# Optimization experiments

Hardware: AMD Instinct MI355X
Metric: run time of the kernel (lower is better)

Reference implementation:

```python
import jax, jax.numpy as jnp
import numpy as np

B, T, C = 4, 2048, 1024
NH = 16
HD = C // NH
ROPE_BASE = 10000.0


def setup_inputs() -> dict:
    key = jax.random.key(0)
    k1, k2, k3, k4, k5 = jax.random.split(key, 5)
    s = 1.0 / np.sqrt(C)
    return {
        "x": jax.random.normal(k1, (B, T, C), dtype=jnp.float32),
        "W_qkv": jax.random.normal(k2, (C, 3 * C), dtype=jnp.float32) * s,
        "b_qkv": jax.random.normal(k3, (3 * C,), dtype=jnp.float32) * 0.02,
        "W_proj": jax.random.normal(k4, (C, C), dtype=jnp.float32) * s,
        "b_proj": jax.random.normal(k5, (C,), dtype=jnp.float32) * 0.02,
    }


def _rotate_half(u):
    u1, u2 = u[..., : HD // 2], u[..., HD // 2 :]
    return jnp.concatenate((-u2, u1), axis=-1)


def _rope_cos_sin(t, dtype):
    # inv_freq: [HD/2]; positions: [T]
    inv_freq = 1.0 / (ROPE_BASE ** (jnp.arange(0, HD, 2, dtype=jnp.float32) / HD))
    pos = jnp.arange(t, dtype=jnp.float32)
    freqs = pos[:, None] * inv_freq[None, :]          # [T, HD/2]
    emb = jnp.concatenate((freqs, freqs), axis=-1)    # [T, HD]
    return jnp.cos(emb).astype(dtype), jnp.sin(emb).astype(dtype)


def reference(x, W_qkv, b_qkv, W_proj, b_proj):
    b, t, c = x.shape
    qkv = x @ W_qkv + b_qkv                           # [B,T,3C]
    q, k, v = jnp.split(qkv, 3, axis=-1)
    # [B,T,C] -> [B,NH,T,HD]
    def to_heads(u):
        return u.reshape(b, t, NH, HD).transpose(0, 2, 1, 3)
    q, k, v = to_heads(q), to_heads(k), to_heads(v)
    cos, sin = _rope_cos_sin(t, x.dtype)              # [T,HD] each; broadcast over B,NH
    q = q * cos + _rotate_half(q) * sin
    k = k * cos + _rotate_half(k) * sin
    att = jnp.einsum("bhqd,bhkd->bhqk", q, k) * (1.0 / np.sqrt(HD))
    causal = jnp.tril(jnp.ones((t, t), dtype=bool))
    att = jnp.where(causal, att, -jnp.inf)
    att = jax.nn.softmax(att, axis=-1)
    y = jnp.einsum("bhqk,bhkd->bhqd", att, v)         # [B,NH,T,HD]
    y = y.transpose(0, 2, 1, 3).reshape(b, t, c)
    return y @ W_proj + b_proj
```

## Files before the change

kernel.cpp:

```cpp
#include <hip/hip_runtime.h>
#include <cstdint>
#include <cstddef>

typedef __attribute__((ext_vector_type(8))) short short8;
typedef __attribute__((ext_vector_type(4))) float float4x;
typedef __attribute__((ext_vector_type(16))) float float16x;
typedef __attribute__((ext_vector_type(2))) unsigned int uint2v;

__device__ __forceinline__ uint16_t f2b(float f){
  uint32_t u = __builtin_bit_cast(uint32_t, f);
  u += 0x7FFFu + ((u >> 16) & 1u);
  return (uint16_t)(u >> 16);
}
__device__ __forceinline__ float b2f(uint16_t h){
  uint32_t u = ((uint32_t)h) << 16;
  return __builtin_bit_cast(float, u);
}
__device__ __forceinline__ float4x zero4(){
  float4x v; v[0]=0.f; v[1]=0.f; v[2]=0.f; v[3]=0.f; return v;
}
__device__ __forceinline__ float16x zero16(){
  float16x v;
#pragma unroll
  for (int i = 0; i < 16; i++) v[i] = 0.f;
  return v;
}
__device__ __forceinline__ uint32_t cvtpk(float lo, float hi){
  uint32_t r;
  asm("v_cvt_pk_bf16_f32 %0, %1, %2" : "=v"(r) : "v"(lo), "v"(hi));
  return r;
}
__device__ __forceinline__ void plswap(uint32_t &a, uint32_t &b){
#if __has_builtin(__builtin_amdgcn_permlane32_swap)
  uint2v r = __builtin_amdgcn_permlane32_swap(a, b, false, false);
  a = r[0]; b = r[1];
#else
  uint32_t a2 = (uint32_t)__shfl_xor((int)a, 32, 64);
  uint32_t b2 = (uint32_t)__shfl_xor((int)b, 32, 64);
  bool lo = ((threadIdx.x & 63) < 32);
  uint32_t an = lo ? a : b2;
  uint32_t bn = lo ? a2 : b;
  a = an; b = bn;
#endif
}
__device__ __forceinline__ float fexp2(float x){
#if __has_builtin(__builtin_amdgcn_exp2f)
  return __builtin_amdgcn_exp2f(x);
#else
  return exp2f(x);
#endif
}
__device__ __forceinline__ void gload16(const uint16_t* g, uint16_t* l){
  __builtin_amdgcn_global_load_lds(
      (const __attribute__((address_space(1))) uint32_t*)g,
      (__attribute__((address_space(3))) uint32_t*)l, 16, 0, 0);
}

__global__ __launch_bounds__(256) void k_prep(const float* __restrict__ x, uint16_t* __restrict__ xb,
                                              const float* __restrict__ Wqkv, uint16_t* __restrict__ wqkvt,
                                              const float* __restrict__ Wproj, uint16_t* __restrict__ wprjt){
  __shared__ float tile[32][33];
  const int bid = blockIdx.x;
  if (bid < 8192){
    int i = bid * 256 + threadIdx.x;
    float4 v = ((const float4*)x)[i];
    ushort4 o;
    o.x = f2b(v.x); o.y = f2b(v.y); o.z = f2b(v.z); o.w = f2b(v.w);
    ((ushort4*)xb)[i] = o;
    return;
  }
  const float* W; uint16_t* Wt; int N, i;
  if (bid < 8192 + 3072){ W = Wqkv;  Wt = wqkvt; N = 3072; i = bid - 8192; }
  else                  { W = Wproj; Wt = wprjt; N = 1024; i = bid - 8192 - 3072; }
  const int K = 1024, nb = N >> 5;
  int k0 = (i / nb) * 32, n0 = (i % nb) * 32;
  int c = threadIdx.x & 31, r0 = threadIdx.x >> 5;
  for (int rr = r0; rr < 32; rr += 8)
    tile[rr][c] = W[(size_t)(k0 + rr) * N + n0 + c];
  __syncthreads();
  for (int rr = r0; rr < 32; rr += 8)
    Wt[(size_t)(n0 + rr) * K + k0 + c] = f2b(tile[c][rr]);
}

__global__ __launch_bounds__(512) void k_gemm_qkv(const uint16_t* __restrict__ A,
                                                  const uint16_t* __restrict__ Bt,
                                                  const float* __restrict__ bias,
                                                  uint16_t* __restrict__ qkv,
                                                  uint16_t* __restrict__ vt){
  __shared__ __align__(16) uint16_t SM[49152];
  const int tid = threadIdx.x, lane = tid & 63, wave = tid >> 6;
  const int wm = wave >> 2, wn = wave & 3;
  const int quad = lane >> 4, l15 = lane & 15;

  const int wg = (blockIdx.x & 7) * 96 + (blockIdx.x >> 3);
  const int by = wg / 12, bx = wg % 12;
  const int m0 = by * 128, n0 = bx * 256;

  const int rsr = tid >> 2;
  const int cg  = (tid & 3) ^ ((tid >> 3) & 3);
  const size_t aRow  = (size_t)(m0 + rsr)       * 1024 + cg * 8;
  const size_t bRow0 = (size_t)(n0 + rsr)       * 1024 + cg * 8;
  const size_t bRow1 = (size_t)(n0 + rsr + 128) * 1024 + cg * 8;
  const int dA = tid * 8, dB0 = tid * 8, dB1 = 4096 + tid * 8;
  const int mc8 = (quad ^ ((l15 >> 1) & 3)) * 8;

  float4x acc[4][4];
#pragma unroll
  for (int i = 0; i < 4; i++)
#pragma unroll
    for (int j = 0; j < 4; j++) acc[i][j] = zero4();

#define STAGE(H) { \
  const int sl_ = (H) & 3; \
  gload16(A  + aRow  + (size_t)(H)*32, &SM[sl_*4096 + dA]); \
  gload16(Bt + bRow0 + (size_t)(H)*32, &SM[16384 + sl_*8192 + dB0]); \
  gload16(Bt + bRow1 + (size_t)(H)*32, &SM[16384 + sl_*8192 + dB1]); }
#define LOADFRAGS(SL) \
  short8 af[4], bf[4]; \
  bf[0] = *(const short8*)&SM[16384 + (SL)*8192 + (wn*64 +  0 + l15)*32 + mc8]; \
  bf[1] = *(const short8*)&SM[16384 + (SL)*8192 + (wn*64 + 16 + l15)*32 + mc8]; \
  bf[2] = *(const short8*)&SM[16384 + (SL)*8192 + (wn*64 + 32 + l15)*32 + mc8]; \
  bf[3] = *(const short8*)&SM[16384 + (SL)*8192 + (wn*64 + 48 + l15)*32 + mc8]; \
  af[0] = *(const short8*)&SM[(SL)*4096 + (wm*64 +  0 + l15)*32 + mc8]; \
  af[1] = *(const short8*)&SM[(SL)*4096 + (wm*64 + 16 + l15)*32 + mc8]; \
  af[2] = *(const short8*)&SM[(SL)*4096 + (wm*64 + 32 + l15)*32 + mc8]; \
  af[3] = *(const short8*)&SM[(SL)*4096 + (wm*64 + 48 + l15)*32 + mc8];
#define MM() { \
  __builtin_amdgcn_s_setprio(1); \
  _Pragma("unroll") \
  for (int mt_ = 0; mt_ < 4; mt_++){ \
    acc[mt_][0] = __builtin_amdgcn_mfma_f32_16x16x32_bf16(af[mt_], bf[0], acc[mt_][0], 0, 0, 0); \
    acc[mt_][1] = __builtin_amdgcn_mfma_f32_16x16x32_bf16(af[mt_], bf[1], acc[mt_][1], 0, 0, 0); \
    acc[mt_][2] = __builtin_amdgcn_mfma_f32_16x16x32_bf16(af[mt_], bf[2], acc[mt_][2], 0, 0, 0); \
    acc[mt_][3] = __builtin_amdgcn_mfma_f32_16x16x32_bf16(af[mt_], bf[3], acc[mt_][3], 0, 0, 0); \
  } \
  __builtin_amdgcn_s_setprio(0); }
#define BAR() \
  __builtin_amdgcn_sched_barrier(0); __builtin_amdgcn_s_barrier(); __builtin_amdgcn_sched_barrier(0);

  STAGE(0) STAGE(1) STAGE(2)
  asm volatile("s_waitcnt vmcnt(6)" ::: "memory");
  BAR();

  for (int p = 0; p < 29; ++p){
    const int sl = p & 3;
    LOADFRAGS(sl)
    STAGE(p + 3)
    MM()
    asm volatile("s_waitcnt vmcnt(6)" ::: "memory");
    BAR();
  }
  {
    LOADFRAGS(1)
    MM()
    asm volatile("s_waitcnt vmcnt(3)" ::: "memory");
    BAR();
  }
  {
    LOADFRAGS(2)
    MM()
    asm volatile("s_waitcnt vmcnt(0)" ::: "memory");
    BAR();
  }
  {
    LOADFRAGS(3)
    MM()
  }
#undef STAGE
#undef LOADFRAGS
#undef MM
#undef BAR

  if (bx < 8){
#pragma unroll
    for (int mt = 0; mt < 4; mt++){
      int grow = m0 + wm*64 + mt*16 + quad*4;
      int tpos = grow & 2047;
#pragma unroll
      for (int nt = 0; nt < 2; nt++){
        int gcol = n0 + wn*64 + nt*16 + l15;
        float bv1 = bias[gcol], bv2 = bias[gcol + 32];
        int i = nt*16 + l15;
        float inv = exp2f(-(float)i * 0.4152410118609203f);
#pragma unroll
        for (int r = 0; r < 4; r++){
          float ang = (float)(tpos + r) * inv;
          float s, c;
          __sincosf(ang, &s, &c);
          float u1 = acc[mt][nt][r]   + bv1;
          float u2 = acc[mt][nt+2][r] + bv2;
          qkv[(size_t)(grow + r)*3072 + gcol]      = f2b(u1*c - u2*s);
          qkv[(size_t)(grow + r)*3072 + gcol + 32] = f2b(u2*c + u1*s);
        }
      }
    }
  } else {
    const int h = (bx - 8)*4 + wn;
    const int bb = m0 >> 11;
    const int tb0 = (m0 & 2047) + wm*64;
    const int bh64 = (bb*16 + h)*64;
    uint16_t* T = &SM[wave*4608];
    const int d32 = lane & 31, th = lane >> 5;
    __syncthreads();
#pragma unroll
    for (int nt = 0; nt < 4; nt++){
      int gcol = n0 + wn*64 + nt*16 + l15;
      float bv = bias[gcol];
#pragma unroll
      for (int mt = 0; mt < 4; mt++)
#pragma unroll
        for (int r = 0; r < 4; r++)
          T[(nt*16 + l15)*72 + mt*16 + quad*4 + r] = f2b(acc[mt][nt][r] + bv);
    }
    __syncthreads();
#pragma unroll
    for (int dd = 0; dd < 2; dd++)
#pragma unroll
      for (int it = 0; it < 4; it++){
        short8 v = *(const short8*)&T[(d32 + 32*dd)*72 + th*32 + it*8];
        *(short8*)&vt[((size_t)(bh64 + d32 + 32*dd))*2048 + tb0 + th*32 + it*8] = v;
      }
  }
}

__global__ __launch_bounds__(256, 3) void k_gemm_proj(const uint16_t* __restrict__ A,
                                                      const uint16_t* __restrict__ Bt,
                                                      const float* __restrict__ bias,
                                                      float* __restrict__ Cout,
                                                      int M, int N, int K){
  __shared__ __align__(16) uint16_t As[2][128*32];
  __shared__ __align__(16) uint16_t Bs[2][128*32];
  const int tid = threadIdx.x, lane = tid & 63, wave = tid >> 6;
  const int wr = wave >> 1, wc = wave & 1;
  const int m0 = blockIdx.y * 128, n0 = blockIdx.x * 128;
  const int quad = lane >> 4, l15 = lane & 15;
  const int rowA = tid >> 2, chA = tid & 3;

  float4x acc[4][4];
  for (int i = 0; i < 4; i++) for (int j = 0; j < 4; j++) acc[i][j] = zero4();

  const uint16_t* pa0 = &A[(size_t)(m0 + rowA)*K + chA*8];
  const uint16_t* pa1 = &A[(size_t)(m0 + rowA + 64)*K + chA*8];
  const uint16_t* pb0 = &Bt[(size_t)(n0 + rowA)*K + chA*8];
  const uint16_t* pb1 = &Bt[(size_t)(n0 + rowA + 64)*K + chA*8];

  gload16(pa0, &As[0][tid*8]);
  gload16(pa1, &As[0][64*32 + tid*8]);
  gload16(pb0, &Bs[0][tid*8]);
  gload16(pb1, &Bs[0][64*32 + tid*8]);

  int buf = 0;
  for (int k0 = 0; k0 < K; k0 += 32){
    __syncthreads();
    if (k0 + 32 < K){
      int nb = buf ^ 1;
      gload16(pa0 + k0 + 32, &As[nb][tid*8]);
      gload16(pa1 + k0 + 32, &As[nb][64*32 + tid*8]);
      gload16(pb0 + k0 + 32, &Bs[nb][tid*8]);
      gload16(pb1 + k0 + 32, &Bs[nb][64*32 + tid*8]);
    }
    short8 af[4], bfr[4];
#pragma unroll
    for (int mt = 0; mt < 4; mt++)
      af[mt] = *(const short8*)&As[buf][(wr*64 + mt*16 + l15)*32 + quad*8];
#pragma unroll
    for (int nt = 0; nt < 4; nt++)
      bfr[nt] = *(const short8*)&Bs[buf][(wc*64 + nt*16 + l15)*32 + quad*8];
#pragma unroll
    for (int mt = 0; mt < 4; mt++)
#pragma unroll
      for (int nt = 0; nt < 4; nt++)
        acc[mt][nt] = __builtin_amdgcn_mfma_f32_16x16x32_bf16(af[mt], bfr[nt], acc[mt][nt], 0, 0, 0);
    buf ^= 1;
  }

#pragma unroll
  for (int mt = 0; mt < 4; mt++){
    int grow = m0 + wr*64 + mt*16 + quad*4;
#pragma unroll
    for (int nt = 0; nt < 4; nt++){
      int gcol = n0 + wc*64 + nt*16 + l15;
      float bv = bias[gcol];
#pragma unroll
      for (int r = 0; r < 4; r++)
        Cout[(size_t)(grow + r)*N + gcol] = acc[mt][nt][r] + bv;
    }
  }
}

__global__ __launch_bounds__(512) void k_attn(const uint16_t* __restrict__ qkv,
                                              const uint16_t* __restrict__ vt,
                                              uint16_t* __restrict__ y){
  __shared__ __align__(16) uint16_t Klds[3][64*64];
  __shared__ __align__(16) uint16_t Vlds[3][64*64];

  const int Did = blockIdx.x;
  const int g = Did & 7, ii = Did >> 3;
  const int bh = g*8 + (ii >> 2);
  const int X  = ii & 3;
  const int b = bh >> 4, h = bh & 15;
  const int lane = threadIdx.x & 63, w = threadIdx.x >> 6;
  const int l31 = lane & 31, hi = lane >> 5;

  const uint16_t* Qbase  = qkv + (size_t)b*2048*3072 + h*64;
  const uint16_t* Kbase  = qkv + (size_t)b*2048*3072 + 1024 + h*64;
  const uint16_t* Vtbase = vt  + (size_t)bh*64*2048;

  const float S2 = 0.18033688011112042f;
  const float M2 = 43.28085122666890f;

  const int isV  = w >> 2;
  const int rbase = (w & 3) * 16;
  const int rsub = lane >> 3, csub = lane & 7;

  const int cA = X, cB = 7 - X;
  const int KT_A = 4*cA + 4;
  const int TS = 36;

  int c = cA;
  int qr = c*256 + w*32;

  short8 aq[4];
#pragma unroll
  for (int kc = 0; kc < 4; kc++)
    aq[kc] = *(const short8*)&Qbase[(size_t)(qr + l31)*3072 + kc*16 + hi*8];

  float16x o[2];
  o[0] = zero16(); o[1] = zero16();
  float lr4[4] = {0.f, 0.f, 0.f, 0.f};

  auto epilogue = [&](){
    float l = (lr4[0] + lr4[1]) + (lr4[2] + lr4[3]);
    l += __shfl_xor(l, 32, 64);
    float linv = 1.f / l;
    float lv[16];
#pragma unroll
    for (int r = 0; r < 16; r++)
      lv[r] = __shfl(linv, (r&3) + 8*(r>>2) + 4*hi, 64);
#pragma unroll
    for (int dt = 0; dt < 2; dt++)
#pragma unroll
      for (int r = 0; r < 16; r++){
        int row = (r&3) + 8*(r>>2) + 4*hi;
        y[((size_t)(b*2048 + qr + row))*1024 + h*64 + dt*32 + l31] = f2b(o[dt][r] * lv[r]);
      }
  };

#define STAGE_KV(TT, SL) { \
  const int kt_ = ((TT) < KT_A) ? (TT) : (TT) - KT_A; \
  _Pragma("unroll") \
  for (int j = 0; j < 2; j++){ \
    int r_  = rbase + j*8 + rsub; \
    int cg_ = csub ^ (r_ & 7); \
    if (isV) gload16(Vtbase + (size_t)r_*2048 + (size_t)kt_*64 + cg_*8, \
                     &Vlds[SL][(rbase + j*8)*64 + lane*8]); \
    else     gload16(Kbase  + (size_t)(kt_*64 + r_)*3072 + cg_*8, \
                     &Klds[SL][(rbase + j*8)*64 + lane*8]); \
  } }
#define ABAR() \
  __builtin_amdgcn_sched_barrier(0); __builtin_amdgcn_s_barrier(); __builtin_amdgcn_sched_barrier(0);

  STAGE_KV(0, 0)
  STAGE_KV(1, 1)
  asm volatile("s_waitcnt vmcnt(2)" ::: "memory");
  ABAR();

  for (int t = 0; t < TS; ++t){
    const int sl = t % 3;
    if (t + 2 < TS) STAGE_KV(t + 2, (t + 2) % 3)

    if (t == KT_A){
      epilogue();
      c = cB; qr = c*256 + w*32;
#pragma unroll
      for (int kc = 0; kc < 4; kc++)
        aq[kc] = *(const short8*)&Qbase[(size_t)(qr + l31)*3072 + kc*16 + hi*8];
      o[0] = zero16(); o[1] = zero16();
      lr4[0] = lr4[1] = lr4[2] = lr4[3] = 0.f;
    }

    const int kt = (t < KT_A) ? t : t - KT_A;
    if (kt*64 <= qr + 31){
      float16x p0 = zero16(), p1 = zero16();
      __builtin_amdgcn_s_setprio(1);
#pragma unroll
      for (int kc = 0; kc < 4; kc++){
        const int ch = 2*kc + hi;
        short8 ak0 = *(const short8*)&Klds[sl][(l31)*64      + ((ch ^ (l31 & 7))*8)];
        short8 ak1 = *(const short8*)&Klds[sl][(32 + l31)*64 + ((ch ^ (l31 & 7))*8)];
        p0 = __builtin_amdgcn_mfma_f32_32x32x16_bf16(ak0, aq[kc], p0, 0, 0, 0);
        p1 = __builtin_amdgcn_mfma_f32_32x32x16_bf16(ak1, aq[kc], p1, 0, 0, 0);
      }
      __builtin_amdgcn_s_setprio(0);

      if (kt*64 + 63 > qr){
        const int tq = qr + l31;
#pragma unroll
        for (int r = 0; r < 16; r++){
          int kb = kt*64 + (r&3) + 8*(r>>2) + 4*hi;
          if (kb > tq)      p0[r] = -1e30f;
          if (kb + 32 > tq) p1[r] = -1e30f;
        }
      }

#pragma unroll
      for (int r = 0; r < 16; r++){
        float e0 = fexp2(__builtin_fmaf(p0[r], S2, -M2));
        float e1 = fexp2(__builtin_fmaf(p1[r], S2, -M2));
        lr4[r & 3] += e0 + e1;
        p0[r] = e0; p1[r] = e1;
      }

      __builtin_amdgcn_s_setprio(1);
#pragma unroll
      for (int kc = 0; kc < 4; kc++){
        const int e8 = (kc & 1)*8;
        uint32_t w0, w1, w2, w3;
        if (kc < 2){
          w0 = cvtpk(p0[e8+0], p0[e8+1]); w1 = cvtpk(p0[e8+2], p0[e8+3]);
          w2 = cvtpk(p0[e8+4], p0[e8+5]); w3 = cvtpk(p0[e8+6], p0[e8+7]);
        } else {
          w0 = cvtpk(p1[e8+0], p1[e8+1]); w1 = cvtpk(p1[e8+2], p1[e8+3]);
          w2 = cvtpk(p1[e8+4], p1[e8+5]); w3 = cvtpk(p1[e8+6], p1[e8+7]);
        }
        plswap(w0, w2);
        plswap(w1, w3);
        union { uint32_t u[4]; short8 s; } ap;
        ap.u[0] = w0; ap.u[1] = w1; ap.u[2] = w2; ap.u[3] = w3;

        const int ch = 2*kc + hi;
        short8 bv0 = *(const short8*)&Vlds[sl][(l31)*64      + ((ch ^ (l31 & 7))*8)];
        short8 bv1 = *(const short8*)&Vlds[sl][(32 + l31)*64 + ((ch ^ (l31 & 7))*8)];
        o[0] = __builtin_amdgcn_mfma_f32_32x32x16_bf16(ap.s, bv0, o[0], 0, 0, 0);
        o[1] = __builtin_amdgcn_mfma_f32_32x32x16_bf16(ap.s, bv1, o[1], 0, 0, 0);
      }
      __builtin_amdgcn_s_setprio(0);
    }

    if (t < TS - 2) asm volatile("s_waitcnt vmcnt(2)" ::: "memory");
    else            asm volatile("s_waitcnt vmcnt(0)" ::: "memory");
    ABAR();
  }
#undef STAGE_KV
#undef ABAR

  epilogue();
}

extern "C" void kernel_launch(void* const* d_in, const int* in_sizes, int n_in,
                              void* d_out, int out_size, void* d_ws, size_t ws_size,
                              hipStream_t stream){
  const float* x     = (const float*)d_in[0];
  const float* Wqkv  = (const float*)d_in[1];
  const float* bqkv  = (const float*)d_in[2];
  const float* Wproj = (const float*)d_in[3];
  const float* bproj = (const float*)d_in[4];

  uint16_t* p = (uint16_t*)d_ws;
  uint16_t* xb    = p; p += (size_t)8192*1024;
  uint16_t* wqkvt = p; p += (size_t)3072*1024;
  uint16_t* wprjt = p; p += (size_t)1024*1024;
  uint16_t* qkv   = p; p += (size_t)8192*3072;
  uint16_t* vt    = p; p += (size_t)64*64*2048;
  uint16_t* yb    = p; p += (size_t)8192*1024;

  k_prep<<<12288, 256, 0, stream>>>(x, xb, Wqkv, wqkvt, Wproj, wprjt);
  k_gemm_qkv<<<768, 512, 0, stream>>>(xb, wqkvt, bqkv, qkv, vt);
  k_attn<<<256, 512, 0, stream>>>(qkv, vt, yb);
  k_gemm_proj<<<dim3(8, 64), 256, 0, stream>>>(yb, wprjt, bproj, (float*)d_out, 8192, 1024, 1024);
}
```

Baseline: 253.2 us.

## Double-buffer LDS fragments in QKV GEMM and port proj GEMM to 4-stage pipeline

```diff
diff --git a/kernel.cpp b/kernel.cpp
--- a/kernel.cpp
+++ b/kernel.cpp
@@ -110,12 +110,162 @@
 #pragma unroll
     for (int j = 0; j < 4; j++) acc[i][j] = zero4();
 
+  short8 afA[4], bfA[4], afB[4], bfB[4];
+
 #define STAGE(H) { \
   const int sl_ = (H) & 3; \
   gload16(A  + aRow  + (size_t)(H)*32, &SM[sl_*4096 + dA]); \
   gload16(Bt + bRow0 + (size_t)(H)*32, &SM[16384 + sl_*8192 + dB0]); \
   gload16(Bt + bRow1 + (size_t)(H)*32, &SM[16384 + sl_*8192 + dB1]); }
-#define LOADFRAGS(SL) \
+#define LOADF(af_, bf_, SL) { \
+  const int sb_ = 16384 + (SL)*8192; const int sa_ = (SL)*4096; \
+  bf_[0] = *(const short8*)&SM[sb_ + (wn*64 +  0 + l15)*32 + mc8]; \
+  bf_[1] = *(const short8*)&SM[sb_ + (wn*64 + 16 + l15)*32 + mc8]; \
+  bf_[2] = *(const short8*)&SM[sb_ + (wn*64 + 32 + l15)*32 + mc8]; \
+  bf_[3] = *(const short8*)&SM[sb_ + (wn*64 + 48 + l15)*32 + mc8]; \
+  af_[0] = *(const short8*)&SM[sa_ + (wm*64 +  0 + l15)*32 + mc8]; \
+  af_[1] = *(const short8*)&SM[sa_ + (wm*64 + 16 + l15)*32 + mc8]; \
+  af_[2] = *(const short8*)&SM[sa_ + (wm*64 + 32 + l15)*32 + mc8]; \
+  af_[3] = *(const short8*)&SM[sa_ + (wm*64 + 48 + l15)*32 + mc8]; }
+#define MMX(af_, bf_) { \
+  __builtin_amdgcn_s_setprio(1); \
+  _Pragma("unroll") \
+  for (int mt_ = 0; mt_ < 4; mt_++){ \
+    acc[mt_][0] = __builtin_amdgcn_mfma_f32_16x16x32_bf16(af_[mt_], bf_[0], acc[mt_][0], 0, 0, 0); \
+    acc[mt_][1] = __builtin_amdgcn_mfma_f32_16x16x32_bf16(af_[mt_], bf_[1], acc[mt_][1], 0, 0, 0); \
+    acc[mt_][2] = __builtin_amdgcn_mfma_f32_16x16x32_bf16(af_[mt_], bf_[2], acc[mt_][2], 0, 0, 0); \
+    acc[mt_][3] = __builtin_amdgcn_mfma_f32_16x16x32_bf16(af_[mt_], bf_[3], acc[mt_][3], 0, 0, 0); \
+  } \
+  __builtin_amdgcn_s_setprio(0); }
+#define BAR() \
+  __builtin_amdgcn_sched_barrier(0); __builtin_amdgcn_s_barrier(); __builtin_amdgcn_sched_barrier(0);
+#define VM3() asm volatile("s_waitcnt vmcnt(3)" ::: "memory");
+
+  STAGE(0) STAGE(1) STAGE(2)
+  VM3(); BAR();
+  LOADF(afA, bfA, 0)
+
+  for (int t = 0; t < 14; ++t){
+    const int pe = 2*t;
+    STAGE(pe + 3)
+    LOADF(afB, bfB, (pe + 1) & 3)
+    MMX(afA, bfA)
+    VM3(); BAR();
+    STAGE(pe + 4)
+    LOADF(afA, bfA, (pe + 2) & 3)
+    MMX(afB, bfB)
+    VM3(); BAR();
+  }
+  {
+    STAGE(31)
+    LOADF(afB, bfB, 1)
+    MMX(afA, bfA)
+    VM3(); BAR();
+  }
+  {
+    LOADF(afA, bfA, 2)
+    MMX(afB, bfB)
+    asm volatile("s_waitcnt vmcnt(0)" ::: "memory");
+    BAR();
+  }
+  {
+    LOADF(afB, bfB, 3)
+    MMX(afA, bfA)
+  }
+  {
+    MMX(afB, bfB)
+  }
+#undef STAGE
+#undef LOADF
+#undef MMX
+#undef BAR
+#undef VM3
+
+  if (bx < 8){
+#pragma unroll
+    for (int mt = 0; mt < 4; mt++){
+      int grow = m0 + wm*64 + mt*16 + quad*4;
+      int tpos = grow & 2047;
+#pragma unroll
+      for (int nt = 0; nt < 2; nt++){
+        int gcol = n0 + wn*64 + nt*16 + l15;
+        float bv1 = bias[gcol], bv2 = bias[gcol + 32];
+        int i = nt*16 + l15;
+        float inv = exp2f(-(float)i * 0.4152410118609203f);
+#pragma unroll
+        for (int r = 0; r < 4; r++){
+          float ang = (float)(tpos + r) * inv;
+          float s, c;
+          __sincosf(ang, &s, &c);
+          float u1 = acc[mt][nt][r]   + bv1;
+          float u2 = acc[mt][nt+2][r] + bv2;
+          qkv[(size_t)(grow + r)*3072 + gcol]      = f2b(u1*c - u2*s);
+          qkv[(size_t)(grow + r)*3072 + gcol + 32] = f2b(u2*c + u1*s);
+        }
+      }
+    }
+  } else {
+    const int h = (bx - 8)*4 + wn;
+    const int bb = m0 >> 11;
+    const int tb0 = (m0 & 2047) + wm*64;
+    const int bh64 = (bb*16 + h)*64;
+    uint16_t* T = &SM[wave*4608];
+    const int d32 = lane & 31, th = lane >> 5;
+    __syncthreads();
+#pragma unroll
+    for (int nt = 0; nt < 4; nt++){
+      int gcol = n0 + wn*64 + nt*16 + l15;
+      float bv = bias[gcol];
+#pragma unroll
+      for (int mt = 0; mt < 4; mt++)
+#pragma unroll
+        for (int r = 0; r < 4; r++)
+          T[(nt*16 + l15)*72 + mt*16 + quad*4 + r] = f2b(acc[mt][nt][r] + bv);
+    }
+    __syncthreads();
+#pragma unroll
+    for (int dd = 0; dd < 2; dd++)
+#pragma unroll
+      for (int it = 0; it < 4; it++){
+        short8 v = *(const short8*)&T[(d32 + 32*dd)*72 + th*32 + it*8];
+        *(short8*)&vt[((size_t)(bh64 + d32 + 32*dd))*2048 + tb0 + th*32 + it*8] = v;
+      }
+  }
+}
+
+__global__ __launch_bounds__(512) void k_gemm_proj(const uint16_t* __restrict__ A,
+                                                   const uint16_t* __restrict__ Bt,
+                                                   const float* __restrict__ bias,
+                                                   float* __restrict__ Cout){
+  __shared__ __align__(16) uint16_t SM[49152];
+  const int tid = threadIdx.x, lane = tid & 63, wave = tid >> 6;
+  const int wm = wave >> 2, wn = wave & 3;
+  const int quad = lane >> 4, l15 = lane & 15;
+
+  const int wg = (blockIdx.x & 7) * 32 + (blockIdx.x >> 3);
+  const int by = wg >> 2, bx = wg & 3;
+  const int m0 = by * 128, n0 = bx * 256;
+
+  const int rsr = tid >> 2;
+  const int cg  = (tid & 3) ^ ((tid >> 3) & 3);
+  const size_t aRow  = (size_t)(m0 + rsr)       * 1024 + cg * 8;
+  const size_t bRow0 = (size_t)(n0 + rsr)       * 1024 + cg * 8;
+  const size_t bRow1 = (size_t)(n0 + rsr + 128) * 1024 + cg * 8;
+  const int dA = tid * 8, dB0 = tid * 8, dB1 = 4096 + tid * 8;
+  const int mc8 = (quad ^ ((l15 >> 1) & 3)) * 8;
+
+  float4x acc[4][4];
+#pragma unroll
+  for (int i = 0; i < 4; i++)
+#pragma unroll
+    for (int j = 0; j < 4; j++) acc[i][j] = zero4();
+
+#define STAGEP(H) { \
+  const int sl_ = (H) & 3; \
+  gload16(A  + aRow  + (size_t)(H)*32, &SM[sl_*4096 + dA]); \
+  gload16(Bt + bRow0 + (size_t)(H)*32, &SM[16384 + sl_*8192 + dB0]); \
+  gload16(Bt + bRow1 + (size_t)(H)*32, &SM[16384 + sl_*8192 + dB1]); }
+#define LOADFP(SL) \
   short8 af[4], bf[4]; \
   bf[0] = *(const short8*)&SM[16384 + (SL)*8192 + (wn*64 +  0 + l15)*32 + mc8]; \
   bf[1] = *(const short8*)&SM[16384 + (SL)*8192 + (wn*64 + 16 + l15)*32 + mc8]; \
@@ -125,7 +275,7 @@
   af[1] = *(const short8*)&SM[(SL)*4096 + (wm*64 + 16 + l15)*32 + mc8]; \
   af[2] = *(const short8*)&SM[(SL)*4096 + (wm*64 + 32 + l15)*32 + mc8]; \
   af[3] = *(const short8*)&SM[(SL)*4096 + (wm*64 + 48 + l15)*32 + mc8];
-#define MM() { \
+#define MMP() { \
   __builtin_amdgcn_s_setprio(1); \
   _Pragma("unroll") \
   for (int mt_ = 0; mt_ < 4; mt_++){ \
@@ -135,155 +285,52 @@
     acc[mt_][3] = __builtin_amdgcn_mfma_f32_16x16x32_bf16(af[mt_], bf[3], acc[mt_][3], 0, 0, 0); \
   } \
   __builtin_amdgcn_s_setprio(0); }
-#define BAR() \
+#define BARP() \
   __builtin_amdgcn_sched_barrier(0); __builtin_amdgcn_s_barrier(); __builtin_amdgcn_sched_barrier(0);
 
-  STAGE(0) STAGE(1) STAGE(2)
+  STAGEP(0) STAGEP(1) STAGEP(2)
   asm volatile("s_waitcnt vmcnt(6)" ::: "memory");
-  BAR();
+  BARP();
 
   for (int p = 0; p < 29; ++p){
     const int sl = p & 3;
-    LOADFRAGS(sl)
-    STAGE(p + 3)
-    MM()
+    LOADFP(sl)
+    STAGEP(p + 3)
+    MMP()
     asm volatile("s_waitcnt vmcnt(6)" ::: "memory");
-    BAR();
-  }
-  {
-    LOADFRAGS(1)
-    MM()
+    BARP();
+  }
+  {
+    LOADFP(1)
+    MMP()
     asm volatile("s_waitcnt vmcnt(3)" ::: "memory");
-    BAR();
-  }
-  {
-    LOADFRAGS(2)
-    MM()
+    BARP();
+  }
+  {
+    LOADFP(2)
+    MMP()
     asm volatile("s_waitcnt vmcnt(0)" ::: "memory");
-    BAR();
-  }
-  {
-    LOADFRAGS(3)
-    MM()
-  }
-#undef STAGE
-#undef LOADFRAGS
-#undef MM
-#undef BAR
-
-  if (bx < 8){
-#pragma unroll
-    for (int mt = 0; mt < 4; mt++){
-      int grow = m0 + wm*64 + mt*16 + quad*4;
-      int tpos = grow & 2047;
-#pragma unroll
-      for (int nt = 0; nt < 2; nt++){
-        int gcol = n0 + wn*64 + nt*16 + l15;
-        float bv1 = bias[gcol], bv2 = bias[gcol + 32];
-        int i = nt*16 + l15;
-        float inv = exp2f(-(float)i * 0.4152410118609203f);
-#pragma unroll
-        for (int r = 0; r < 4; r++){
-          float ang = (float)(tpos + r) * inv;
-          float s, c;
-          __sincosf(ang, &s, &c);
-          float u1 = acc[mt][nt][r]   + bv1;
-          float u2 = acc[mt][nt+2][r] + bv2;
-          qkv[(size_t)(grow + r)*3072 + gcol]      = f2b(u1*c - u2*s);
-          qkv[(size_t)(grow + r)*3072 + gcol + 32] = f2b(u2*c + u1*s);
-        }
-      }
-    }
-  } else {
-    const int h = (bx - 8)*4 + wn;
-    const int bb = m0 >> 11;
-    const int tb0 = (m0 & 2047) + wm*64;
-    const int bh64 = (bb*16 + h)*64;
-    uint16_t* T = &SM[wave*4608];
-    const int d32 = lane & 31, th = lane >> 5;
-    __syncthreads();
+    BARP();
+  }
+  {
+    LOADFP(3)
+    MMP()
+  }
+#undef STAGEP
+#undef LOADFP
+#undef MMP
+#undef BARP
+
+#pragma unroll
+  for (int mt = 0; mt < 4; mt++){
+    int grow = m0 + wm*64 + mt*16 + quad*4;
 #pragma unroll
     for (int nt = 0; nt < 4; nt++){
       int gcol = n0 + wn*64 + nt*16 + l15;
       float bv = bias[gcol];
 #pragma unroll
-      for (int mt = 0; mt < 4; mt++)
-#pragma unroll
-        for (int r = 0; r < 4; r++)
-          T[(nt*16 + l15)*72 + mt*16 + quad*4 + r] = f2b(acc[mt][nt][r] + bv);
-    }
-    __syncthreads();
-#pragma unroll
-    for (int dd = 0; dd < 2; dd++)
-#pragma unroll
-      for (int it = 0; it < 4; it++){
-        short8 v = *(const short8*)&T[(d32 + 32*dd)*72 + th*32 + it*8];
-        *(short8*)&vt[((size_t)(bh64 + d32 + 32*dd))*2048 + tb0 + th*32 + it*8] = v;
-      }
-  }
-}
-
-__global__ __launch_bounds__(256, 3) void k_gemm_proj(const uint16_t* __restrict__ A,
-                                                      const uint16_t* __restrict__ Bt,
-                                                      const float* __restrict__ bias,
-                                                      float* __restrict__ Cout,
-                                                      int M, int N, int K){
-  __shared__ __align__(16) uint16_t As[2][128*32];
-  __shared__ __align__(16) uint16_t Bs[2][128*32];
-  const int tid = threadIdx.x, lane = tid & 63, wave = tid >> 6;
-  const int wr = wave >> 1, wc = wave & 1;
-  const int m0 = blockIdx.y * 128, n0 = blockIdx.x * 128;
-  const int quad = lane >> 4, l15 = lane & 15;
-  const int rowA = tid >> 2, chA = tid & 3;
-
-  float4x acc[4][4];
-  for (int i = 0; i < 4; i++) for (int j = 0; j < 4; j++) acc[i][j] = zero4();
-
-  const uint16_t* pa0 = &A[(size_t)(m0 + rowA)*K + chA*8];
-  const uint16_t* pa1 = &A[(size_t)(m0 + rowA + 64)*K + chA*8];
-  const uint16_t* pb0 = &Bt[(size_t)(n0 + rowA)*K + chA*8];
-  const uint16_t* pb1 = &Bt[(size_t)(n0 + rowA + 64)*K + chA*8];
-
-  gload16(pa0, &As[0][tid*8]);
-  gload16(pa1, &As[0][64*32 + tid*8]);
-  gload16(pb0, &Bs[0][tid*8]);
-  gload16(pb1, &Bs[0][64*32 + tid*8]);
-
-  int buf = 0;
-  for (int k0 = 0; k0 < K; k0 += 32){
-    __syncthreads();
-    if (k0 + 32 < K){
-      int nb = buf ^ 1;
-      gload16(pa0 + k0 + 32, &As[nb][tid*8]);
-      gload16(pa1 + k0 + 32, &As[nb][64*32 + tid*8]);
-      gload16(pb0 + k0 + 32, &Bs[nb][tid*8]);
-      gload16(pb1 + k0 + 32, &Bs[nb][64*32 + tid*8]);
-    }
-    short8 af[4], bfr[4];
-#pragma unroll
-    for (int mt = 0; mt < 4; mt++)
-      af[mt] = *(const short8*)&As[buf][(wr*64 + mt*16 + l15)*32 + quad*8];
-#pragma unroll
-    for (int nt = 0; nt < 4; nt++)
-      bfr[nt] = *(const short8*)&Bs[buf][(wc*64 + nt*16 + l15)*32 + quad*8];
-#pragma unroll
-    for (int mt = 0; mt < 4; mt++)
-#pragma unroll
-      for (int nt = 0; nt < 4; nt++)
-        acc[mt][nt] = __builtin_amdgcn_mfma_f32_16x16x32_bf16(af[mt], bfr[nt], acc[mt][nt], 0, 0, 0);
-    buf ^= 1;
-  }
-
-#pragma unroll
-  for (int mt = 0; mt < 4; mt++){
-    int grow = m0 + wr*64 + mt*16 + quad*4;
-#pragma unroll
-    for (int nt = 0; nt < 4; nt++){
-      int gcol = n0 + wc*64 + nt*16 + l15;
-      float bv = bias[gcol];
-#pragma unroll
       for (int r = 0; r < 4; r++)
-        Cout[(size_t)(grow + r)*N + gcol] = acc[mt][nt][r] + bv;
+        Cout[(size_t)(grow + r)*1024 + gcol] = acc[mt][nt][r] + bv;
     }
   }
 }
@@ -467,5 +514,5 @@
   k_prep<<<12288, 256, 0, stream>>>(x, xb, Wqkv, wqkvt, Wproj, wprjt);
   k_gemm_qkv<<<768, 512, 0, stream>>>(xb, wqkvt, bqkv, qkv, vt);
   k_attn<<<256, 512, 0, stream>>>(qkv, vt, yb);
-  k_gemm_proj<<<dim3(8, 64), 256, 0, stream>>>(yb, wprjt, bproj, (float*)d_out, 8192, 1024, 1024);
-}
+  k_gemm_proj<<<256, 512, 0, stream>>>(yb, wprjt, bproj, (float*)d_out);
+}
```

Measured after the change: 250.4 us. Within noise of the previous version (-1.1%).
